# Optimization experiments

Hardware: AMD Instinct MI355X
Metric: run time of the kernel (lower is better)

The kernel has to match this reference:

```python
import jax, jax.numpy as jnp
import numpy as np

CD_STEPS = 10  # cd_steps from __init__


def setup_inputs() -> dict:
    key = jax.random.key(0)
    k1, k2, k3, k4 = jax.random.split(key, 4)
    inputs = jax.random.uniform(k1, (8192, 4096), jnp.float32)          # visible units in [0,1]
    w = 0.01 * jax.random.normal(k2, (4096, 64), jnp.float32)           # [num_inputs, num_hidden]
    vb = 0.01 * jax.random.normal(k3, (4096,), jnp.float32)             # visible bias
    hb = 0.01 * jax.random.normal(k4, (64,), jnp.float32)               # hidden bias
    return {"inputs": inputs, "w": w, "vb": vb, "hb": hb}


def _sample_binary(p, key):
    # relu(sign(p - U)) == 1 iff p > U, else 0 (sign(0) -> 0 -> relu -> 0)
    u = jax.random.uniform(key, p.shape, p.dtype)
    return (p > u).astype(p.dtype)


def reference(inputs, w, vb, hb):
    """SemiSupervisedRBM._unlabeled_loss: k-step CD Gibbs chain + free-energy gap."""
    key = jax.random.key(42)

    def cond_h_given_v(v):
        return jax.nn.sigmoid(v @ w + hb)          # [B, H]

    def cond_v_given_h(h):
        return jax.nn.sigmoid(h @ w.T + vb)        # [B, V]

    # initial hidden sample from the data
    h = _sample_binary(cond_h_given_v(inputs), jax.random.fold_in(key, 0))

    def gibbs_step(carry, k):
        h, _ = carry
        kv, kh = jax.random.split(k)
        v = _sample_binary(cond_v_given_h(h), kv)
        h = _sample_binary(cond_h_given_v(v), kh)
        return (h, v), None

    keys = jax.random.split(jax.random.fold_in(key, 1), CD_STEPS)
    (h, v), _ = jax.lax.scan(gibbs_step, (h, inputs), keys)
    v_sample = jax.lax.stop_gradient(v)

    def free_energy(v):
        # -(sum_j softplus(hb + v W)_j + v . vb)
        cond_term = jnp.sum(jax.nn.softplus(v @ w + hb), axis=1)  # [B]
        bias_term = v @ vb                                        # [B]
        return -(cond_term + bias_term)

    return jnp.sum(free_energy(inputs) - free_energy(v_sample))
```

## Files before the change

kernel.cpp:

```cpp
#include <hip/hip_runtime.h>
#include <stdint.h>

typedef __bf16 bf16x8 __attribute__((ext_vector_type(8)));
typedef float f32x4 __attribute__((ext_vector_type(4)));

#define NSTEP 10
#define HALF_V 16777216u
#define HALF_H 262144u

struct TFKeys {
  uint32_t kh0_0, kh0_1;
  uint32_t kv0[NSTEP], kv1[NSTEP];
  uint32_t khs0[NSTEP], khs1[NSTEP];
};

#define TF_ROUND(r) { x0 += x1; x1 = (x1 << (r)) | (x1 >> (32 - (r))); x1 ^= x0; }

__host__ __device__ __forceinline__ void tf2x32(uint32_t k0, uint32_t k1,
    uint32_t x0, uint32_t x1, uint32_t& o0, uint32_t& o1) {
  const uint32_t k2 = k0 ^ k1 ^ 0x1BD11BDAu;
  x0 += k0; x1 += k1;
  TF_ROUND(13) TF_ROUND(15) TF_ROUND(26) TF_ROUND(6)
  x0 += k1; x1 += k2 + 1u;
  TF_ROUND(17) TF_ROUND(29) TF_ROUND(16) TF_ROUND(24)
  x0 += k2; x1 += k0 + 2u;
  TF_ROUND(13) TF_ROUND(15) TF_ROUND(26) TF_ROUND(6)
  x0 += k0; x1 += k1 + 3u;
  TF_ROUND(17) TF_ROUND(29) TF_ROUND(16) TF_ROUND(24)
  x0 += k1; x1 += k2 + 4u;
  TF_ROUND(13) TF_ROUND(15) TF_ROUND(26) TF_ROUND(6)
  x0 += k2; x1 += k0 + 5u;
  o0 = x0; o1 = x1;
}

__device__ __forceinline__ float tf_uniform(uint32_t bits) {
  return __uint_as_float((bits >> 9) | 0x3F800000u) - 1.0f;
}

__device__ __forceinline__ float sigmoidf_(float x) {
  return 1.0f / (1.0f + __expf(-x));
}

__device__ __forceinline__ float softplusf_(float x) {
  return fmaxf(x, 0.0f) + log1pf(__expf(-fabsf(x)));
}

__device__ __forceinline__ unsigned short f2bf(float f) {
  uint32_t u = __float_as_uint(f);
  uint32_t r = (u + 0x7FFFu + ((u >> 16) & 1u)) >> 16;
  return (unsigned short)r;
}

__device__ __forceinline__ bf16x8 as8(uint4 u) { return __builtin_bit_cast(bf16x8, u); }

__global__ void prep_w(const float* __restrict__ w,
                       unsigned short* __restrict__ w_hi, unsigned short* __restrict__ w_lo,
                       unsigned short* __restrict__ wt_hi, unsigned short* __restrict__ wt_lo) {
  int t = blockIdx.x * 256 + threadIdx.x;
  int i = t >> 6, j = t & 63;
  float f = w[t];
  unsigned short hi = f2bf(f);
  float fh = __uint_as_float((uint32_t)hi << 16);
  unsigned short lo = f2bf(f - fh);
  w_hi[t] = hi;             w_lo[t] = lo;
  wt_hi[j * 4096 + i] = hi; wt_lo[j * 4096 + i] = lo;
}

template<int MODE>
__device__ __forceinline__ void h_tail(int wv, int l, int b0, uint32_t k0, uint32_t k1,
    float& acc_fe, const float (*Xp)[64][8], const float* hb_lds,
    unsigned short (*h_lds)[72]) {
  const int cc  = (wv * 64 + l) * 2;
  const int rlo = cc >> 6;
  const int j0  = cc & 63;
  #pragma unroll
  for (int s = 0; s < 2; ++s) {
    const int jj = j0 + s;
    f32x4 pa = *(const f32x4*)&Xp[rlo][jj][0];
    f32x4 pb = *(const f32x4*)&Xp[rlo][jj][4];
    f32x4 qa = *(const f32x4*)&Xp[rlo + 16][jj][0];
    f32x4 qb = *(const f32x4*)&Xp[rlo + 16][jj][4];
    float hbv = hb_lds[jj];
    float xlo = (((pa[0] + pa[1]) + (pa[2] + pa[3]))
               + ((pb[0] + pb[1]) + (pb[2] + pb[3]))) + hbv;
    float xhi = (((qa[0] + qa[1]) + (qa[2] + qa[3]))
               + ((qb[0] + qb[1]) + (qb[2] + qb[3]))) + hbv;
    if (MODE == 2) {
      acc_fe += softplusf_(xlo) + softplusf_(xhi);
    } else {
      if (MODE == 0) acc_fe -= softplusf_(xlo) + softplusf_(xhi);
      uint32_t e0 = (uint32_t)(b0 + rlo) * 64u + (uint32_t)jj;
      uint32_t o0, o1;
      tf2x32(k0, k1, e0, e0 + HALF_H, o0, o1);
      h_lds[rlo][jj]      = (sigmoidf_(xlo) > tf_uniform(o0)) ? (unsigned short)0x3F80 : (unsigned short)0;
      h_lds[16 + rlo][jj] = (sigmoidf_(xhi) > tf_uniform(o1)) ? (unsigned short)0x3F80 : (unsigned short)0;
    }
  }
}

__global__ __launch_bounds__(512, 2)
void rbm_chain(const float* __restrict__ inputs, const float* __restrict__ vb,
               const float* __restrict__ hb,
               const unsigned short* __restrict__ w_hi, const unsigned short* __restrict__ w_lo,
               const unsigned short* __restrict__ wt_hi, const unsigned short* __restrict__ wt_lo,
               float* __restrict__ partial, TFKeys K) {
  __shared__ unsigned short v_lds[8][32][72];
  __shared__ float Xp[32][64][8];
  __shared__ unsigned short h_lds[32][72];
  __shared__ float vb_lds[4096];
  __shared__ float hb_lds[64];
  __shared__ float red[8];

  const int tid = threadIdx.x;
  const int wv  = tid >> 6;
  const int l   = tid & 63;
  const int lg  = l >> 4;
  const int lr  = l & 15;
  const int b0  = blockIdx.x * 16;
  const int colbase = wv * 512;

  for (int u = tid; u < 1024; u += 512)
    ((float4*)vb_lds)[u] = ((const float4*)vb)[u];
  if (tid < 64) hb_lds[tid] = hb[tid];
  __syncthreads();

  float acc_fe = 0.0f;
  f32x4 accx[2][4];
  #pragma unroll
  for (int rt = 0; rt < 2; ++rt)
    #pragma unroll
    for (int ct = 0; ct < 4; ++ct) accx[rt][ct] = f32x4{0.f, 0.f, 0.f, 0.f};

  #pragma unroll 1
  for (int sc = 0; sc < 8; ++sc) {
    const int base = colbase + sc * 64;
    #pragma unroll
    for (int u = 0; u < 8; ++u) {
      int idx = u * 64 + l;
      int row = idx >> 4, f4 = idx & 15;
      int grow = (row < 16) ? (b0 + row) : (4096 + b0 + row - 16);
      float4 x = *(const float4*)(inputs + (size_t)grow * 4096 + base + f4 * 4);
      int cg = base + f4 * 4;
      acc_fe -= x.x * vb_lds[cg] + x.y * vb_lds[cg + 1]
              + x.z * vb_lds[cg + 2] + x.w * vb_lds[cg + 3];
      ushort4 h4;
      h4.x = f2bf(x.x); h4.y = f2bf(x.y); h4.z = f2bf(x.z); h4.w = f2bf(x.w);
      *(ushort4*)&v_lds[wv][row][f4 * 4] = h4;
    }
    #pragma unroll
    for (int ks = 0; ks < 2; ++ks) {
      const int kg = base + ks * 32;
      bf16x8 A0 = as8(*(const uint4*)&v_lds[wv][lr][ks * 32 + lg * 8]);
      bf16x8 A1 = as8(*(const uint4*)&v_lds[wv][16 + lr][ks * 32 + lg * 8]);
      #pragma unroll
      for (int ct = 0; ct < 4; ++ct) {
        size_t wo = (size_t)(ct * 16 + lr) * 4096 + kg + lg * 8;
        bf16x8 bh = as8(*(const uint4*)(wt_hi + wo));
        bf16x8 bl = as8(*(const uint4*)(wt_lo + wo));
        accx[0][ct] = __builtin_amdgcn_mfma_f32_16x16x32_bf16(A0, bh, accx[0][ct], 0, 0, 0);
        accx[0][ct] = __builtin_amdgcn_mfma_f32_16x16x32_bf16(A0, bl, accx[0][ct], 0, 0, 0);
        accx[1][ct] = __builtin_amdgcn_mfma_f32_16x16x32_bf16(A1, bh, accx[1][ct], 0, 0, 0);
        accx[1][ct] = __builtin_amdgcn_mfma_f32_16x16x32_bf16(A1, bl, accx[1][ct], 0, 0, 0);
      }
    }
  }
  #pragma unroll
  for (int rt = 0; rt < 2; ++rt)
    #pragma unroll
    for (int ct = 0; ct < 4; ++ct)
      #pragma unroll
      for (int q = 0; q < 4; ++q)
        Xp[rt * 16 + lg * 4 + q][ct * 16 + lr][wv] = accx[rt][ct][q];
  __syncthreads();
  h_tail<0>(wv, l, b0, K.kh0_0, K.kh0_1, acc_fe, Xp, hb_lds, h_lds);
  __syncthreads();

  for (int step = 0; step < NSTEP; ++step) {
    const uint32_t kv0 = K.kv0[step], kv1 = K.kv1[step];
    const bool last = (step == NSTEP - 1);

    bf16x8 ha00 = as8(*(const uint4*)&h_lds[lr][lg * 8]);
    bf16x8 ha01 = as8(*(const uint4*)&h_lds[lr][32 + lg * 8]);
    bf16x8 ha10 = as8(*(const uint4*)&h_lds[16 + lr][lg * 8]);
    bf16x8 ha11 = as8(*(const uint4*)&h_lds[16 + lr][32 + lg * 8]);

    #pragma unroll
    for (int rt = 0; rt < 2; ++rt)
      #pragma unroll
      for (int ct = 0; ct < 4; ++ct) accx[rt][ct] = f32x4{0.f, 0.f, 0.f, 0.f};

    #pragma unroll 1
    for (int sc = 0; sc < 8; ++sc) {
      const int base = colbase + sc * 64;
      #pragma unroll
      for (int t = 0; t < 4; ++t) {
        const int ig = base + t * 16 + lr;
        const uint4* wh = (const uint4*)(w_hi + (size_t)ig * 64);
        const uint4* wl = (const uint4*)(w_lo + (size_t)ig * 64);
        bf16x8 bh0 = as8(wh[lg]);
        bf16x8 bh1 = as8(wh[4 + lg]);
        bf16x8 bl0 = as8(wl[lg]);
        bf16x8 bl1 = as8(wl[4 + lg]);
        f32x4 a0 = {0.f, 0.f, 0.f, 0.f}, a1 = {0.f, 0.f, 0.f, 0.f};
        a0 = __builtin_amdgcn_mfma_f32_16x16x32_bf16(ha00, bh0, a0, 0, 0, 0);
        a0 = __builtin_amdgcn_mfma_f32_16x16x32_bf16(ha01, bh1, a0, 0, 0, 0);
        a0 = __builtin_amdgcn_mfma_f32_16x16x32_bf16(ha00, bl0, a0, 0, 0, 0);
        a0 = __builtin_amdgcn_mfma_f32_16x16x32_bf16(ha01, bl1, a0, 0, 0, 0);
        a1 = __builtin_amdgcn_mfma_f32_16x16x32_bf16(ha10, bh0, a1, 0, 0, 0);
        a1 = __builtin_amdgcn_mfma_f32_16x16x32_bf16(ha11, bh1, a1, 0, 0, 0);
        a1 = __builtin_amdgcn_mfma_f32_16x16x32_bf16(ha10, bl0, a1, 0, 0, 0);
        a1 = __builtin_amdgcn_mfma_f32_16x16x32_bf16(ha11, bl1, a1, 0, 0, 0);
        const float vbv  = vb_lds[ig];
        const float vbva = last ? vbv : 0.0f;
        #pragma unroll
        for (int q = 0; q < 4; ++q) {
          const int rit = lg * 4 + q;
          float x0 = a0[q] + vbv, x1 = a1[q] + vbv;
          uint32_t e0 = (uint32_t)(b0 + rit) * 4096u + (uint32_t)ig;
          uint32_t o0, o1;
          tf2x32(kv0, kv1, e0, e0 + HALF_V, o0, o1);
          bool s0 = sigmoidf_(x0) > tf_uniform(o0);
          bool s1 = sigmoidf_(x1) > tf_uniform(o1);
          v_lds[wv][rit][t * 16 + lr]      = s0 ? (unsigned short)0x3F80 : (unsigned short)0;
          v_lds[wv][16 + rit][t * 16 + lr] = s1 ? (unsigned short)0x3F80 : (unsigned short)0;
          acc_fe += (s0 ? vbva : 0.0f) + (s1 ? vbva : 0.0f);
        }
      }
      #pragma unroll
      for (int ks = 0; ks < 2; ++ks) {
        const int kg = base + ks * 32;
        bf16x8 A0 = as8(*(const uint4*)&v_lds[wv][lr][ks * 32 + lg * 8]);
        bf16x8 A1 = as8(*(const uint4*)&v_lds[wv][16 + lr][ks * 32 + lg * 8]);
        #pragma unroll
        for (int ct = 0; ct < 4; ++ct) {
          size_t wo = (size_t)(ct * 16 + lr) * 4096 + kg + lg * 8;
          bf16x8 bh = as8(*(const uint4*)(wt_hi + wo));
          bf16x8 bl = as8(*(const uint4*)(wt_lo + wo));
          accx[0][ct] = __builtin_amdgcn_mfma_f32_16x16x32_bf16(A0, bh, accx[0][ct], 0, 0, 0);
          accx[0][ct] = __builtin_amdgcn_mfma_f32_16x16x32_bf16(A0, bl, accx[0][ct], 0, 0, 0);
          accx[1][ct] = __builtin_amdgcn_mfma_f32_16x16x32_bf16(A1, bh, accx[1][ct], 0, 0, 0);
          accx[1][ct] = __builtin_amdgcn_mfma_f32_16x16x32_bf16(A1, bl, accx[1][ct], 0, 0, 0);
        }
      }
    }

    #pragma unroll
    for (int rt = 0; rt < 2; ++rt)
      #pragma unroll
      for (int ct = 0; ct < 4; ++ct)
        #pragma unroll
        for (int q = 0; q < 4; ++q)
          Xp[rt * 16 + lg * 4 + q][ct * 16 + lr][wv] = accx[rt][ct][q];
    __syncthreads();
    if (last) h_tail<2>(wv, l, b0, 0u, 0u, acc_fe, Xp, hb_lds, h_lds);
    else      h_tail<1>(wv, l, b0, K.khs0[step], K.khs1[step], acc_fe, Xp, hb_lds, h_lds);
    __syncthreads();
  }

  float v = acc_fe;
  #pragma unroll
  for (int off = 32; off; off >>= 1) v += __shfl_down(v, off);
  if (l == 0) red[wv] = v;
  __syncthreads();
  if (tid == 0) {
    float s = 0.f;
    #pragma unroll
    for (int i = 0; i < 8; ++i) s += red[i];
    partial[blockIdx.x] = s;
  }
}

__global__ void finish_reduce(const float* __restrict__ partial, float* __restrict__ out) {
  __shared__ float r[4];
  float v = partial[threadIdx.x];
  #pragma unroll
  for (int off = 32; off; off >>= 1) v += __shfl_down(v, off);
  if ((threadIdx.x & 63) == 0) r[threadIdx.x >> 6] = v;
  __syncthreads();
  if (threadIdx.x == 0) out[0] = r[0] + r[1] + r[2] + r[3];
}

extern "C" void kernel_launch(void* const* d_in, const int* in_sizes, int n_in,
                              void* d_out, int out_size, void* d_ws, size_t ws_size,
                              hipStream_t stream) {
  const float* inputs = (const float*)d_in[0];
  const float* w      = (const float*)d_in[1];
  const float* vb     = (const float*)d_in[2];
  const float* hb     = (const float*)d_in[3];
  float* out = (float*)d_out;

  unsigned short* w_hi  = (unsigned short*)d_ws;
  unsigned short* w_lo  = (unsigned short*)((char*)d_ws + (512u << 10));
  unsigned short* wt_hi = (unsigned short*)((char*)d_ws + (1024u << 10));
  unsigned short* wt_lo = (unsigned short*)((char*)d_ws + (1536u << 10));
  float* partial        = (float*)((char*)d_ws + (2048u << 10));

  TFKeys K;
  uint32_t kc0, kc1;
  tf2x32(0u, 42u, 0u, 0u, K.kh0_0, K.kh0_1);
  tf2x32(0u, 42u, 0u, 1u, kc0, kc1);
  uint32_t A[NSTEP], B[NSTEP], flat[2 * NSTEP];
  for (int i = 0; i < NSTEP; ++i) tf2x32(kc0, kc1, (uint32_t)i, (uint32_t)(NSTEP + i), A[i], B[i]);
  for (int i = 0; i < NSTEP; ++i) { flat[i] = A[i]; flat[NSTEP + i] = B[i]; }
  for (int t = 0; t < NSTEP; ++t) {
    uint32_t key0 = flat[2 * t], key1 = flat[2 * t + 1];
    uint32_t C0, D0, C1, D1;
    tf2x32(key0, key1, 0u, 2u, C0, D0);
    tf2x32(key0, key1, 1u, 3u, C1, D1);
    K.kv0[t] = C0; K.kv1[t] = C1;
    K.khs0[t] = D0; K.khs1[t] = D1;
  }

  prep_w<<<1024, 256, 0, stream>>>(w, w_hi, w_lo, wt_hi, wt_lo);
  rbm_chain<<<256, 512, 0, stream>>>(inputs, vb, hb, w_hi, w_lo, wt_hi, wt_lo, partial, K);
  finish_reduce<<<1, 256, 0, stream>>>(partial, out);
}
```

Baseline: 905.9 us.

## Halve rows per block, double grid, shrink LDS, and cheapen sampling math

Each block now handles 16 rows (8 data pairs) instead of 32, so the grid doubles to 512 blocks and launch bounds allow 4 blocks per SM, aiming for more occupancy. The visible-bias LDS copy is dropped in favour of global reads, and the partial-sum layout is changed to a padded row-major Xp. Sampling uses a division-free sigmoid comparison and alignbit rotations in Threefry, and the visible bias is folded into the MFMA accumulator initialisation. In exchange, each block re-reads the weight matrix for fewer rows, which doubles total weight traffic.

```diff
diff --git a/kernel.cpp b/kernel.cpp
--- a/kernel.cpp
+++ b/kernel.cpp
@@ -7,6 +7,7 @@
 #define NSTEP 10
 #define HALF_V 16777216u
 #define HALF_H 262144u
+#define XPS 516
 
 struct TFKeys {
   uint32_t kh0_0, kh0_1;
@@ -14,7 +15,15 @@
   uint32_t khs0[NSTEP], khs1[NSTEP];
 };
 
-#define TF_ROUND(r) { x0 += x1; x1 = (x1 << (r)) | (x1 >> (32 - (r))); x1 ^= x0; }
+__host__ __device__ __forceinline__ uint32_t rotl_(uint32_t x, uint32_t r) {
+#ifdef __HIP_DEVICE_COMPILE__
+  return __builtin_amdgcn_alignbit(x, x, 32u - r);
+#else
+  return (x << r) | (x >> (32u - r));
+#endif
+}
+
+#define TF_ROUND(r) { x0 += x1; x1 = rotl_(x1, (r)); x1 ^= x0; }
 
 __host__ __device__ __forceinline__ void tf2x32(uint32_t k0, uint32_t k1,
     uint32_t x0, uint32_t x1, uint32_t& o0, uint32_t& o1) {
@@ -37,12 +46,12 @@
   return __uint_as_float((bits >> 9) | 0x3F800000u) - 1.0f;
 }
 
-__device__ __forceinline__ float sigmoidf_(float x) {
-  return 1.0f / (1.0f + __expf(-x));
-}
-
 __device__ __forceinline__ float softplusf_(float x) {
   return fmaxf(x, 0.0f) + log1pf(__expf(-fabsf(x)));
+}
+
+__device__ __forceinline__ bool sig_gt(float x, float u) {
+  return fmaf(u, __expf(-x), u) < 1.0f;
 }
 
 __device__ __forceinline__ unsigned short f2bf(float f) {
@@ -67,47 +76,100 @@
 }
 
 template<int MODE>
-__device__ __forceinline__ void h_tail(int wv, int l, int b0, uint32_t k0, uint32_t k1,
-    float& acc_fe, const float (*Xp)[64][8], const float* hb_lds,
-    unsigned short (*h_lds)[72]) {
-  const int cc  = (wv * 64 + l) * 2;
-  const int rlo = cc >> 6;
-  const int j0  = cc & 63;
-  #pragma unroll
-  for (int s = 0; s < 2; ++s) {
-    const int jj = j0 + s;
-    f32x4 pa = *(const f32x4*)&Xp[rlo][jj][0];
-    f32x4 pb = *(const f32x4*)&Xp[rlo][jj][4];
-    f32x4 qa = *(const f32x4*)&Xp[rlo + 16][jj][0];
-    f32x4 qb = *(const f32x4*)&Xp[rlo + 16][jj][4];
-    float hbv = hb_lds[jj];
-    float xlo = (((pa[0] + pa[1]) + (pa[2] + pa[3]))
-               + ((pb[0] + pb[1]) + (pb[2] + pb[3]))) + hbv;
-    float xhi = (((qa[0] + qa[1]) + (qa[2] + qa[3]))
-               + ((qb[0] + qb[1]) + (qb[2] + qb[3]))) + hbv;
-    if (MODE == 2) {
-      acc_fe += softplusf_(xlo) + softplusf_(xhi);
-    } else {
-      if (MODE == 0) acc_fe -= softplusf_(xlo) + softplusf_(xhi);
-      uint32_t e0 = (uint32_t)(b0 + rlo) * 64u + (uint32_t)jj;
-      uint32_t o0, o1;
-      tf2x32(k0, k1, e0, e0 + HALF_H, o0, o1);
-      h_lds[rlo][jj]      = (sigmoidf_(xlo) > tf_uniform(o0)) ? (unsigned short)0x3F80 : (unsigned short)0;
-      h_lds[16 + rlo][jj] = (sigmoidf_(xhi) > tf_uniform(o1)) ? (unsigned short)0x3F80 : (unsigned short)0;
+__device__ __forceinline__ void h_tail(int p, int j, int b0, uint32_t k0, uint32_t k1,
+    float& acc_fe, const float* Xp, const float* hb_lds, unsigned short (*h_lds)[72]) {
+  const float* xl = Xp + (2 * p) * XPS + j;
+  const float* xh = Xp + (2 * p + 1) * XPS + j;
+  float s0 = 0.f, s1 = 0.f;
+  #pragma unroll
+  for (int w = 0; w < 8; ++w) { s0 += xl[w * 64]; s1 += xh[w * 64]; }
+  float hbv = hb_lds[j];
+  float xlo = s0 + hbv, xhi = s1 + hbv;
+  if (MODE == 2) { acc_fe += softplusf_(xlo) + softplusf_(xhi); return; }
+  if (MODE == 0) acc_fe -= softplusf_(xlo) + softplusf_(xhi);
+  uint32_t e0 = (uint32_t)(b0 + p) * 64u + (uint32_t)j;
+  uint32_t o0, o1;
+  tf2x32(k0, k1, e0, e0 + HALF_H, o0, o1);
+  h_lds[2 * p][j]     = sig_gt(xlo, tf_uniform(o0)) ? (unsigned short)0x3F80 : (unsigned short)0;
+  h_lds[2 * p + 1][j] = sig_gt(xhi, tf_uniform(o1)) ? (unsigned short)0x3F80 : (unsigned short)0;
+}
+
+template<bool LAST>
+__device__ __forceinline__ void gibbs_step(
+    int wv, int l, int lg, int lr, int b0, int colbase,
+    uint32_t kv0, uint32_t kv1, uint32_t kh0, uint32_t kh1,
+    const unsigned short* __restrict__ w_hi, const unsigned short* __restrict__ w_lo,
+    const unsigned short* __restrict__ wt_hi, const unsigned short* __restrict__ wt_lo,
+    const float* __restrict__ vb,
+    unsigned short (*v_lds)[16][72], unsigned short (*h_lds)[72],
+    float* Xp, const float* hb_lds, float& acc_fe)
+{
+  bf16x8 ha0 = as8(*(const uint4*)&h_lds[lr][lg * 8]);
+  bf16x8 ha1 = as8(*(const uint4*)&h_lds[lr][32 + lg * 8]);
+  f32x4 accx[4];
+  #pragma unroll
+  for (int ct = 0; ct < 4; ++ct) accx[ct] = f32x4{0.f, 0.f, 0.f, 0.f};
+
+  #pragma unroll 1
+  for (int sc = 0; sc < 8; ++sc) {
+    const int base = colbase + sc * 64;
+    #pragma unroll
+    for (int t = 0; t < 4; ++t) {
+      const int ig = base + t * 16 + lr;
+      const uint4* wh = (const uint4*)(w_hi + (size_t)ig * 64);
+      const uint4* wl = (const uint4*)(w_lo + (size_t)ig * 64);
+      uint4 bh0 = wh[lg], bh1 = wh[4 + lg];
+      uint4 bl0 = wl[lg], bl1 = wl[4 + lg];
+      const float vbv = vb[ig];
+      uint32_t c0 = (uint32_t)(b0 + 2 * lg) * 4096u + (uint32_t)ig;
+      uint32_t oA0, oA1, oB0, oB1;
+      tf2x32(kv0, kv1, c0, c0 + HALF_V, oA0, oA1);
+      tf2x32(kv0, kv1, c0 + 4096u, c0 + 4096u + HALF_V, oB0, oB1);
+      f32x4 a = {vbv, vbv, vbv, vbv};
+      a = __builtin_amdgcn_mfma_f32_16x16x32_bf16(ha0, as8(bh0), a, 0, 0, 0);
+      a = __builtin_amdgcn_mfma_f32_16x16x32_bf16(ha1, as8(bh1), a, 0, 0, 0);
+      a = __builtin_amdgcn_mfma_f32_16x16x32_bf16(ha0, as8(bl0), a, 0, 0, 0);
+      a = __builtin_amdgcn_mfma_f32_16x16x32_bf16(ha1, as8(bl1), a, 0, 0, 0);
+      const uint32_t bits[4] = {oA0, oA1, oB0, oB1};
+      #pragma unroll
+      for (int q = 0; q < 4; ++q) {
+        bool s = sig_gt(a[q], tf_uniform(bits[q]));
+        v_lds[wv][4 * lg + q][t * 16 + lr] = s ? (unsigned short)0x3F80 : (unsigned short)0;
+        if (LAST) acc_fe += s ? vbv : 0.0f;
+      }
     }
-  }
-}
-
-__global__ __launch_bounds__(512, 2)
+    #pragma unroll
+    for (int ks = 0; ks < 2; ++ks) {
+      const int kg = base + ks * 32;
+      bf16x8 A0 = as8(*(const uint4*)&v_lds[wv][lr][ks * 32 + lg * 8]);
+      #pragma unroll
+      for (int ct = 0; ct < 4; ++ct) {
+        size_t wo = (size_t)(ct * 16 + lr) * 4096 + kg + lg * 8;
+        accx[ct] = __builtin_amdgcn_mfma_f32_16x16x32_bf16(A0, as8(*(const uint4*)(wt_hi + wo)), accx[ct], 0, 0, 0);
+        accx[ct] = __builtin_amdgcn_mfma_f32_16x16x32_bf16(A0, as8(*(const uint4*)(wt_lo + wo)), accx[ct], 0, 0, 0);
+      }
+    }
+  }
+  #pragma unroll
+  for (int ct = 0; ct < 4; ++ct)
+    #pragma unroll
+    for (int q = 0; q < 4; ++q)
+      Xp[(4 * lg + q) * XPS + wv * 64 + ct * 16 + lr] = accx[ct][q];
+  __syncthreads();
+  if (LAST) h_tail<2>(wv, l, b0, 0u, 0u, acc_fe, Xp, hb_lds, h_lds);
+  else      h_tail<1>(wv, l, b0, kh0, kh1, acc_fe, Xp, hb_lds, h_lds);
+  __syncthreads();
+}
+
+__global__ __launch_bounds__(512, 4)
 void rbm_chain(const float* __restrict__ inputs, const float* __restrict__ vb,
                const float* __restrict__ hb,
                const unsigned short* __restrict__ w_hi, const unsigned short* __restrict__ w_lo,
                const unsigned short* __restrict__ wt_hi, const unsigned short* __restrict__ wt_lo,
                float* __restrict__ partial, TFKeys K) {
-  __shared__ unsigned short v_lds[8][32][72];
-  __shared__ float Xp[32][64][8];
-  __shared__ unsigned short h_lds[32][72];
-  __shared__ float vb_lds[4096];
+  __shared__ unsigned short v_lds[8][16][72];
+  __shared__ unsigned short h_lds[16][72];
+  __shared__ float Xp[16 * XPS];
   __shared__ float hb_lds[64];
   __shared__ float red[8];
 
@@ -116,146 +178,62 @@
   const int l   = tid & 63;
   const int lg  = l >> 4;
   const int lr  = l & 15;
-  const int b0  = blockIdx.x * 16;
+  const int b0  = blockIdx.x * 8;
   const int colbase = wv * 512;
 
-  for (int u = tid; u < 1024; u += 512)
-    ((float4*)vb_lds)[u] = ((const float4*)vb)[u];
   if (tid < 64) hb_lds[tid] = hb[tid];
-  __syncthreads();
 
   float acc_fe = 0.0f;
-  f32x4 accx[2][4];
-  #pragma unroll
-  for (int rt = 0; rt < 2; ++rt)
-    #pragma unroll
-    for (int ct = 0; ct < 4; ++ct) accx[rt][ct] = f32x4{0.f, 0.f, 0.f, 0.f};
-
-  #pragma unroll 1
-  for (int sc = 0; sc < 8; ++sc) {
-    const int base = colbase + sc * 64;
-    #pragma unroll
-    for (int u = 0; u < 8; ++u) {
-      int idx = u * 64 + l;
-      int row = idx >> 4, f4 = idx & 15;
-      int grow = (row < 16) ? (b0 + row) : (4096 + b0 + row - 16);
-      float4 x = *(const float4*)(inputs + (size_t)grow * 4096 + base + f4 * 4);
-      int cg = base + f4 * 4;
-      acc_fe -= x.x * vb_lds[cg] + x.y * vb_lds[cg + 1]
-              + x.z * vb_lds[cg + 2] + x.w * vb_lds[cg + 3];
-      ushort4 h4;
-      h4.x = f2bf(x.x); h4.y = f2bf(x.y); h4.z = f2bf(x.z); h4.w = f2bf(x.w);
-      *(ushort4*)&v_lds[wv][row][f4 * 4] = h4;
-    }
-    #pragma unroll
-    for (int ks = 0; ks < 2; ++ks) {
-      const int kg = base + ks * 32;
-      bf16x8 A0 = as8(*(const uint4*)&v_lds[wv][lr][ks * 32 + lg * 8]);
-      bf16x8 A1 = as8(*(const uint4*)&v_lds[wv][16 + lr][ks * 32 + lg * 8]);
-      #pragma unroll
-      for (int ct = 0; ct < 4; ++ct) {
-        size_t wo = (size_t)(ct * 16 + lr) * 4096 + kg + lg * 8;
-        bf16x8 bh = as8(*(const uint4*)(wt_hi + wo));
-        bf16x8 bl = as8(*(const uint4*)(wt_lo + wo));
-        accx[0][ct] = __builtin_amdgcn_mfma_f32_16x16x32_bf16(A0, bh, accx[0][ct], 0, 0, 0);
-        accx[0][ct] = __builtin_amdgcn_mfma_f32_16x16x32_bf16(A0, bl, accx[0][ct], 0, 0, 0);
-        accx[1][ct] = __builtin_amdgcn_mfma_f32_16x16x32_bf16(A1, bh, accx[1][ct], 0, 0, 0);
-        accx[1][ct] = __builtin_amdgcn_mfma_f32_16x16x32_bf16(A1, bl, accx[1][ct], 0, 0, 0);
-      }
-    }
-  }
-  #pragma unroll
-  for (int rt = 0; rt < 2; ++rt)
-    #pragma unroll
-    for (int ct = 0; ct < 4; ++ct)
-      #pragma unroll
-      for (int q = 0; q < 4; ++q)
-        Xp[rt * 16 + lg * 4 + q][ct * 16 + lr][wv] = accx[rt][ct][q];
-  __syncthreads();
-  h_tail<0>(wv, l, b0, K.kh0_0, K.kh0_1, acc_fe, Xp, hb_lds, h_lds);
-  __syncthreads();
-
-  for (int step = 0; step < NSTEP; ++step) {
-    const uint32_t kv0 = K.kv0[step], kv1 = K.kv1[step];
-    const bool last = (step == NSTEP - 1);
-
-    bf16x8 ha00 = as8(*(const uint4*)&h_lds[lr][lg * 8]);
-    bf16x8 ha01 = as8(*(const uint4*)&h_lds[lr][32 + lg * 8]);
-    bf16x8 ha10 = as8(*(const uint4*)&h_lds[16 + lr][lg * 8]);
-    bf16x8 ha11 = as8(*(const uint4*)&h_lds[16 + lr][32 + lg * 8]);
-
-    #pragma unroll
-    for (int rt = 0; rt < 2; ++rt)
-      #pragma unroll
-      for (int ct = 0; ct < 4; ++ct) accx[rt][ct] = f32x4{0.f, 0.f, 0.f, 0.f};
-
+
+  {
+    f32x4 accx[4];
+    #pragma unroll
+    for (int ct = 0; ct < 4; ++ct) accx[ct] = f32x4{0.f, 0.f, 0.f, 0.f};
     #pragma unroll 1
     for (int sc = 0; sc < 8; ++sc) {
       const int base = colbase + sc * 64;
       #pragma unroll
-      for (int t = 0; t < 4; ++t) {
-        const int ig = base + t * 16 + lr;
-        const uint4* wh = (const uint4*)(w_hi + (size_t)ig * 64);
-        const uint4* wl = (const uint4*)(w_lo + (size_t)ig * 64);
-        bf16x8 bh0 = as8(wh[lg]);
-        bf16x8 bh1 = as8(wh[4 + lg]);
-        bf16x8 bl0 = as8(wl[lg]);
-        bf16x8 bl1 = as8(wl[4 + lg]);
-        f32x4 a0 = {0.f, 0.f, 0.f, 0.f}, a1 = {0.f, 0.f, 0.f, 0.f};
-        a0 = __builtin_amdgcn_mfma_f32_16x16x32_bf16(ha00, bh0, a0, 0, 0, 0);
-        a0 = __builtin_amdgcn_mfma_f32_16x16x32_bf16(ha01, bh1, a0, 0, 0, 0);
-        a0 = __builtin_amdgcn_mfma_f32_16x16x32_bf16(ha00, bl0, a0, 0, 0, 0);
-        a0 = __builtin_amdgcn_mfma_f32_16x16x32_bf16(ha01, bl1, a0, 0, 0, 0);
-        a1 = __builtin_amdgcn_mfma_f32_16x16x32_bf16(ha10, bh0, a1, 0, 0, 0);
-        a1 = __builtin_amdgcn_mfma_f32_16x16x32_bf16(ha11, bh1, a1, 0, 0, 0);
-        a1 = __builtin_amdgcn_mfma_f32_16x16x32_bf16(ha10, bl0, a1, 0, 0, 0);
-        a1 = __builtin_amdgcn_mfma_f32_16x16x32_bf16(ha11, bl1, a1, 0, 0, 0);
-        const float vbv  = vb_lds[ig];
-        const float vbva = last ? vbv : 0.0f;
-        #pragma unroll
-        for (int q = 0; q < 4; ++q) {
-          const int rit = lg * 4 + q;
-          float x0 = a0[q] + vbv, x1 = a1[q] + vbv;
-          uint32_t e0 = (uint32_t)(b0 + rit) * 4096u + (uint32_t)ig;
-          uint32_t o0, o1;
-          tf2x32(kv0, kv1, e0, e0 + HALF_V, o0, o1);
-          bool s0 = sigmoidf_(x0) > tf_uniform(o0);
-          bool s1 = sigmoidf_(x1) > tf_uniform(o1);
-          v_lds[wv][rit][t * 16 + lr]      = s0 ? (unsigned short)0x3F80 : (unsigned short)0;
-          v_lds[wv][16 + rit][t * 16 + lr] = s1 ? (unsigned short)0x3F80 : (unsigned short)0;
-          acc_fe += (s0 ? vbva : 0.0f) + (s1 ? vbva : 0.0f);
-        }
+      for (int u = 0; u < 4; ++u) {
+        int idx = u * 64 + l;
+        int m = idx >> 4, f4 = idx & 15;
+        int phys = b0 + (m >> 1) + ((m & 1) << 12);
+        float4 x  = *(const float4*)(inputs + (size_t)phys * 4096 + base + f4 * 4);
+        float4 vv = *(const float4*)(vb + base + f4 * 4);
+        acc_fe -= x.x * vv.x + x.y * vv.y + x.z * vv.z + x.w * vv.w;
+        ushort4 h4;
+        h4.x = f2bf(x.x); h4.y = f2bf(x.y); h4.z = f2bf(x.z); h4.w = f2bf(x.w);
+        *(ushort4*)&v_lds[wv][m][f4 * 4] = h4;
       }
       #pragma unroll
       for (int ks = 0; ks < 2; ++ks) {
         const int kg = base + ks * 32;
         bf16x8 A0 = as8(*(const uint4*)&v_lds[wv][lr][ks * 32 + lg * 8]);
-        bf16x8 A1 = as8(*(const uint4*)&v_lds[wv][16 + lr][ks * 32 + lg * 8]);
         #pragma unroll
         for (int ct = 0; ct < 4; ++ct) {
           size_t wo = (size_t)(ct * 16 + lr) * 4096 + kg + lg * 8;
-          bf16x8 bh = as8(*(const uint4*)(wt_hi + wo));
-          bf16x8 bl = as8(*(const uint4*)(wt_lo + wo));
-          accx[0][ct] = __builtin_amdgcn_mfma_f32_16x16x32_bf16(A0, bh, accx[0][ct], 0, 0, 0);
-          accx[0][ct] = __builtin_amdgcn_mfma_f32_16x16x32_bf16(A0, bl, accx[0][ct], 0, 0, 0);
-          accx[1][ct] = __builtin_amdgcn_mfma_f32_16x16x32_bf16(A1, bh, accx[1][ct], 0, 0, 0);
-          accx[1][ct] = __builtin_amdgcn_mfma_f32_16x16x32_bf16(A1, bl, accx[1][ct], 0, 0, 0);
+          accx[ct] = __builtin_amdgcn_mfma_f32_16x16x32_bf16(A0, as8(*(const uint4*)(wt_hi + wo)), accx[ct], 0, 0, 0);
+          accx[ct] = __builtin_amdgcn_mfma_f32_16x16x32_bf16(A0, as8(*(const uint4*)(wt_lo + wo)), accx[ct], 0, 0, 0);
         }
       }
     }
-
-    #pragma unroll
-    for (int rt = 0; rt < 2; ++rt)
-      #pragma unroll
-      for (int ct = 0; ct < 4; ++ct)
-        #pragma unroll
-        for (int q = 0; q < 4; ++q)
-          Xp[rt * 16 + lg * 4 + q][ct * 16 + lr][wv] = accx[rt][ct][q];
+    #pragma unroll
+    for (int ct = 0; ct < 4; ++ct)
+      #pragma unroll
+      for (int q = 0; q < 4; ++q)
+        Xp[(4 * lg + q) * XPS + wv * 64 + ct * 16 + lr] = accx[ct][q];
     __syncthreads();
-    if (last) h_tail<2>(wv, l, b0, 0u, 0u, acc_fe, Xp, hb_lds, h_lds);
-    else      h_tail<1>(wv, l, b0, K.khs0[step], K.khs1[step], acc_fe, Xp, hb_lds, h_lds);
+    h_tail<0>(wv, l, b0, K.kh0_0, K.kh0_1, acc_fe, Xp, hb_lds, h_lds);
     __syncthreads();
   }
+
+  #pragma unroll 1
+  for (int step = 0; step < NSTEP - 1; ++step)
+    gibbs_step<false>(wv, l, lg, lr, b0, colbase,
+                      K.kv0[step], K.kv1[step], K.khs0[step], K.khs1[step],
+                      w_hi, w_lo, wt_hi, wt_lo, vb, v_lds, h_lds, Xp, hb_lds, acc_fe);
+  gibbs_step<true>(wv, l, lg, lr, b0, colbase,
+                   K.kv0[NSTEP - 1], K.kv1[NSTEP - 1], 0u, 0u,
+                   w_hi, w_lo, wt_hi, wt_lo, vb, v_lds, h_lds, Xp, hb_lds, acc_fe);
 
   float v = acc_fe;
   #pragma unroll
@@ -271,13 +249,18 @@
 }
 
 __global__ void finish_reduce(const float* __restrict__ partial, float* __restrict__ out) {
-  __shared__ float r[4];
+  __shared__ float r[8];
   float v = partial[threadIdx.x];
   #pragma unroll
   for (int off = 32; off; off >>= 1) v += __shfl_down(v, off);
   if ((threadIdx.x & 63) == 0) r[threadIdx.x >> 6] = v;
   __syncthreads();
-  if (threadIdx.x == 0) out[0] = r[0] + r[1] + r[2] + r[3];
+  if (threadIdx.x == 0) {
+    float s = 0.f;
+    #pragma unroll
+    for (int i = 0; i < 8; ++i) s += r[i];
+    out[0] = s;
+  }
 }
 
 extern "C" void kernel_launch(void* const* d_in, const int* in_sizes, int n_in,
@@ -312,6 +295,6 @@
   }
 
   prep_w<<<1024, 256, 0, stream>>>(w, w_hi, w_lo, wt_hi, wt_lo);
-  rbm_chain<<<256, 512, 0, stream>>>(inputs, vb, hb, w_hi, w_lo, wt_hi, wt_lo, partial, K);
-  finish_reduce<<<1, 256, 0, stream>>>(partial, out);
-}
+  rbm_chain<<<512, 512, 0, stream>>>(inputs, vb, hb, w_hi, w_lo, wt_hi, wt_lo, partial, K);
+  finish_reduce<<<1, 512, 0, stream>>>(partial, out);
+}
```

Result: slower. 1.384 ms (+52.8%).
